# Performance work log

Measured on AMD Instinct MI355X. Metric: run time of the kernel, lower is better.

## Reference

```python
import jax, jax.numpy as jnp
import numpy as np

N_USER = 805   # herbs
N_ITEM = 390   # symptoms
N = 1195       # total nodes
D = 64         # embedding_dim (forced by final matmul)
E = 1_000_000
E_SUB = 500_000
B = 2048
BN_EPS = 1e-5


def _gcn(x, W, b, edge):
    # GCNConv_SH: message = Linear(x_j), aggr='mean', then tanh.
    # Linear commutes with mean (bias included when in-degree>0; isolated nodes -> 0),
    # so transform nodes once, then gather->segment-mean.
    h = x @ W.T + b                      # [N, D]
    src, dst = edge[0], edge[1]
    agg = jax.ops.segment_sum(h[src], dst, num_segments=N)          # [N, D]
    cnt = jax.ops.segment_sum(jnp.ones(edge.shape[1], x.dtype), dst, num_segments=N)
    mean = agg / jnp.maximum(cnt, 1.0)[:, None]   # isolated nodes stay 0 (PyG mean aggr)
    return jnp.tanh(mean)


def _two_layer(x, W1, b1, W2, b2, edge):
    return _gcn(_gcn(x, W1, b1, edge), W2, b2, edge)


def _norm(x, axis):
    # self.Norm(emb, count, n_dim): L2 normalize along n_dim (0 for user side, 1 for item side)
    return x / jnp.linalg.norm(x, axis=axis, keepdims=True)


def setup_inputs() -> dict:
    key = jax.random.key(0)
    ks = jax.random.split(key, 12)
    emb = jax.random.normal(ks[0], (N, D), jnp.float32)
    s = 1.0 / np.sqrt(D)
    W1 = jax.random.normal(ks[1], (D, D), jnp.float32) * s
    b1 = jnp.zeros((D,), jnp.float32)
    W2 = jax.random.normal(ks[2], (D, D), jnp.float32) * s
    b2 = jnp.zeros((D,), jnp.float32)
    mlp_W = jax.random.normal(ks[3], (64, D), jnp.float32) * s
    mlp_b = jnp.zeros((64,), jnp.float32)
    bn_gamma = jnp.ones((64,), jnp.float32)
    bn_beta = jnp.zeros((64,), jnp.float32)
    # multi-hot prescription; guarantee nonzero row sums for the mean-pool divide
    presc = (jax.random.uniform(ks[4], (B, N_ITEM)) < 0.05).astype(jnp.float32)
    presc = presc.at[:, 0].set(1.0)
    total_g = jax.random.randint(ks[5], (2, E), 0, N)
    sub_g1 = jax.random.randint(ks[6], (2, E_SUB), 0, N)
    sub_g2 = jax.random.randint(ks[7], (2, E_SUB), 0, N)
    edge_index_SH = jax.random.randint(ks[8], (2, 1000), 0, N)
    return {"edge_index_SH": edge_index_SH, "prescription": presc,
            "emb": emb, "W1": W1, "b1": b1, "W2": W2, "b2": b2,
            "mlp_W": mlp_W, "mlp_b": mlp_b, "bn_gamma": bn_gamma, "bn_beta": bn_beta,
            "total_g": total_g, "sub_g1": sub_g1, "sub_g2": sub_g2}


def reference(edge_index_SH, prescription, emb, W1, b1, W2, b2, mlp_W, mlp_b,
              bn_gamma, bn_beta, total_g, sub_g1, sub_g2):
    # edge_index_SH is accepted (forward signature) but unused, as in the source.
    x_SH1 = emb                                   # SH_embedding(arange(1195))
    x_SH6 = _two_layer(emb, W1, b1, W2, b2, total_g)   # two shared GCNConv_SH layers
    SH_g3 = _two_layer(emb, W1, b1, W2, b2, sub_g1)
    SH_g33 = _two_layer(emb, W1, b1, W2, b2, sub_g2)

    # ssl_layer_loss returns normalized previous (raw-embedding) views
    s_u = _norm(x_SH1[:N_USER], 0)   # [805, D]
    s_i = _norm(x_SH1[N_USER:], 1)   # [390, D]
    # sgl_loss returns normalized sub-graph-1 views
    n_u = _norm(SH_g3[:N_USER], 0)
    n_i = _norm(SH_g3[N_USER:], 1)
    # Same2Loss (reconstructed): fuse all contrastive views into final node reps
    c_u = 0.25 * (s_i + n_i + _norm(x_SH6[N_USER:], 1) + _norm(SH_g33[N_USER:], 1))  # [390, D]
    c_i = 0.25 * (s_u + n_u + _norm(x_SH6[:N_USER], 0) + _norm(SH_g33[:N_USER], 0))  # [805, D]

    e_synd = prescription @ c_u                           # [B, D]
    e_synd = e_synd / prescription.sum(axis=1, keepdims=True)
    h = e_synd @ mlp_W.T + mlp_b                          # [B, 64]
    mu = h.mean(axis=0)
    var = h.var(axis=0)                                   # biased, as torch BN training
    h = (h - mu) / jnp.sqrt(var + BN_EPS) * bn_gamma + bn_beta
    h = jax.nn.relu(h)
    pre = h @ c_i.T                                       # [B, 805]
    return pre
```

## Files before the change

kernel.cpp:

```cpp
#include <hip/hip_runtime.h>
#include <hip/hip_bf16.h>


#define NN    1195
#define NUSER 805
#define NITEM 390
#define DD    64
#define BB    2048
#define NPAD  1216
#define E_TOT 1000000
#define E_SUB 500000
#define MT    19
#define KT    8
#define CHUNK 3
#define LSTR  72
#define OUT2STRIDE (NN*DD)
#define CPG    299
#define P8W    152
#define FNT    13
#define KPAD   448
#define ENT    7

typedef unsigned int uint;
typedef unsigned short u16;
typedef unsigned char u8;
typedef __attribute__((ext_vector_type(8))) short short8;
typedef __attribute__((ext_vector_type(4))) float f32x4;

__device__ __forceinline__ float wsum(float v) {
#pragma unroll
    for (int m = 32; m > 0; m >>= 1) v += __shfl_xor(v, m, 64);
    return v;
}
__device__ __forceinline__ u16 f2b(float f) {
    uint u = __float_as_uint(f);
    return (u16)((u + 0x7FFFu + ((u >> 16) & 1u)) >> 16);
}
__device__ __forceinline__ float b2f16(u16 b) { return __uint_as_float(((uint)b) << 16); }
__device__ __forceinline__ void split4(const float* v, u16* hh, u16* ll) {
#pragma unroll
    for (int j = 0; j < 4; ++j) {
        u16 h = f2b(v[j]);
        hh[j] = h;
        ll[j] = f2b(v[j] - b2f16(h));
    }
}
__device__ __forceinline__ uint2 pack4(const u16* x) {
    uint2 o;
    o.x = (uint)x[0] | ((uint)x[1] << 16);
    o.y = (uint)x[2] | ((uint)x[3] << 16);
    return o;
}

#define CVT_EMB   0
#define CVT_W1    76480
#define CVT_B1    80576
#define CVT_W2    80640
#define CVT_B2    84736
#define CVT_MLPW  84800
#define CVT_MLPB  88896
#define CVT_GAMMA 88960
#define CVT_BETA  89024
#define CVT_TOTAL 89088

constexpr size_t alignUp64(size_t x) { return (x + 63) & ~size_t(63); }
constexpr size_t OFF_BNS  = 0;
constexpr size_t OFF_CNSS = 128;
constexpr size_t OFF_FLAG = 384;
constexpr size_t OFF_CVT  = 448;
constexpr size_t OFF_ABF  = alignUp64(OFF_CVT + CVT_TOTAL);
constexpr size_t OFF_RC   = alignUp64(OFF_ABF + (3ull * NN * NPAD) / 2);
constexpr size_t OFF_POOL = alignUp64(OFF_RC + 3ull * NPAD);


__global__ __launch_bounds__(1024, 8) void k_front(const void* presc, const void* emb,
        const void* p1, const void* p2, const void* p3, const void* p4,
        const void* p5, const void* p6, const void* p7, const void* p8, const void* p9,
        const int* __restrict__ tg, const int* __restrict__ s1, const int* __restrict__ s2,
        float* __restrict__ dst, float* __restrict__ cnss, float* __restrict__ bnsum,
        int* __restrict__ flag, uint* __restrict__ P8,
        int S0, int S1, int R, int rows, int HB) {
    extern __shared__ __align__(16) uint lds[];
    int b = blockIdx.x, t = threadIdx.x;
    int isbf = (((const u16*)presc)[0] == 0x3F80u) ? 1 : 0;
    if (b < HB) {
        int RS0 = R * S0, RS1 = R * S1;
        int g, p, r;
        if (b < RS0)            { g = 0; p = b % S0; r = b / S0; }
        else if (b < RS0 + RS1) { int b2 = b - RS0;        g = 1; p = b2 % S1; r = b2 / S1; }
        else                    { int b3 = b - RS0 - RS1;  g = 2; p = b3 % S1; r = b3 / S1; }
        int Sg = g ? S1 : S0;
        int cb = (g == 0) ? 0 : S0 + (g - 1) * S1;
        int r0 = r * rows;
        int nw4 = (rows * P8W) >> 2;
        {
            uint4* l4 = (uint4*)lds;
            for (int i = t; i < nw4; i += 1024) l4[i] = (uint4){0u, 0u, 0u, 0u};
        }
        __syncthreads();
        const int* eg = (g == 0) ? tg : (g == 1 ? s1 : s2);
        int Eg = (g == 0) ? E_TOT : E_SUB;
        int e0 = (int)(((long)p * Eg / Sg) & ~3L);
        int e1 = (p == Sg - 1) ? Eg : (int)(((long)(p + 1) * Eg / Sg) & ~3L);
        const int* srcp = eg;
        const int* dstp = eg + Eg;
        for (int i = e0 + t * 4; i < e1; i += 1024 * 4) {
            int4 d4 = *(const int4*)(dstp + i);
            int4 s4 = *(const int4*)(srcp + i);
            int rw;
            rw = d4.x - r0; if ((unsigned)rw < (unsigned)rows) atomicAdd(&lds[rw * P8W + (s4.x >> 3)], 1u << ((s4.x & 7) * 4));
            rw = d4.y - r0; if ((unsigned)rw < (unsigned)rows) atomicAdd(&lds[rw * P8W + (s4.y >> 3)], 1u << ((s4.y & 7) * 4));
            rw = d4.z - r0; if ((unsigned)rw < (unsigned)rows) atomicAdd(&lds[rw * P8W + (s4.z >> 3)], 1u << ((s4.z & 7) * 4));
            rw = d4.w - r0; if ((unsigned)rw < (unsigned)rows) atomicAdd(&lds[rw * P8W + (s4.w >> 3)], 1u << ((s4.w & 7) * 4));
        }
        __syncthreads();
        int rmax = rows; if (r0 + rmax > NN) rmax = NN - r0;
        uint* out = P8 + ((size_t)(cb + p) * NN + r0) * P8W;
        int n4 = (rmax * P8W) >> 2;
        const uint4* l4 = (const uint4*)lds;
        uint4* o4 = (uint4*)out;
        for (int i = t; i < n4; i += 1024) o4[i] = l4[i];
    } else if (b == HB) {
        if (t < 192) cnss[64 + t] = 0.0f;
        if (t < 128) bnsum[t] = 0.0f;
        int c = t & 63, chunk = t >> 6;
        float s = 0.0f;
        const u16* e16 = (const u16*)emb;
        const float* e32 = (const float*)emb;
        for (int r = chunk; r < NUSER; r += 16) {
            float v = isbf ? b2f16(e16[r * 64 + c]) : e32[r * 64 + c];
            s = fmaf(v, v, s);
        }
        float* sd = (float*)lds;
        sd[t] = s;
        __syncthreads();
        if (t < 64) {
            float tot = 0.0f;
#pragma unroll
            for (int j = 0; j < 16; ++j) tot += sd[j * 64 + t];
            cnss[t] = tot;
        }
    } else {
        int i = (b - HB - 1) * 1024 + t;
        if (i == 0) *flag = isbf;
        if (i < CVT_TOTAL) {
            const void* s2p; int o2;
            if      (i < CVT_W1)    { s2p = p1; o2 = i; }
            else if (i < CVT_B1)    { s2p = p2; o2 = i - CVT_W1; }
            else if (i < CVT_W2)    { s2p = p3; o2 = i - CVT_B1; }
            else if (i < CVT_B2)    { s2p = p4; o2 = i - CVT_W2; }
            else if (i < CVT_MLPW)  { s2p = p5; o2 = i - CVT_B2; }
            else if (i < CVT_MLPB)  { s2p = p6; o2 = i - CVT_MLPW; }
            else if (i < CVT_GAMMA) { s2p = p7; o2 = i - CVT_MLPB; }
            else if (i < CVT_BETA)  { s2p = p8; o2 = i - CVT_GAMMA; }
            else                    { s2p = p9; o2 = i - CVT_BETA; }
            dst[i] = isbf ? __bfloat162float(((const __hip_bfloat16*)s2p)[o2])
                          : ((const float*)s2p)[o2];
        }
    }
}

__device__ __forceinline__ void xf2_body(int g, int n0, int t,
        const float* xsrc, size_t xgstride,
        const float* part, const float* rcnt, int fromPart, int rowlim,
        const float* W, const float* bias,
        u16* Hhi, u16* Hlo, size_t hgstride, int ostride,
        u16* Ah, u16* Al, u16* Bh, u16* Bl, float* bs) {
    int w = t >> 6, l = t & 63;
    if (t < 64) bs[t] = bias ? bias[t] : 0.0f;
    int r = t >> 2, c0 = (t & 3) * 16;
    {
        const float* Wr = W + r * 64 + c0;
        float av[16];
#pragma unroll
        for (int j4 = 0; j4 < 4; ++j4) {
            float4 v = *(const float4*)(Wr + j4 * 4);
            av[j4*4+0] = v.x; av[j4*4+1] = v.y; av[j4*4+2] = v.z; av[j4*4+3] = v.w;
        }
#pragma unroll
        for (int j4 = 0; j4 < 4; ++j4) {
            u16 hh[4], ll[4];
            split4(av + j4*4, hh, ll);
            *(uint2*)(Ah + r * LSTR + c0 + j4*4) = pack4(hh);
            *(uint2*)(Al + r * LSTR + c0 + j4*4) = pack4(ll);
        }
    }
    {
        int node = n0 + r;
        float xr[16];
#pragma unroll
        for (int j = 0; j < 16; ++j) xr[j] = 0.0f;
        if (node < rowlim) {
            if (fromPart) {
#pragma unroll
                for (int k = 0; k < KT; ++k) {
                    const float* pp = part + (((size_t)k * 3 + g) * NPAD + node) * 64 + c0;
#pragma unroll
                    for (int j4 = 0; j4 < 4; ++j4) {
                        float4 v = *(const float4*)(pp + j4 * 4);
                        xr[j4*4+0] += v.x; xr[j4*4+1] += v.y;
                        xr[j4*4+2] += v.z; xr[j4*4+3] += v.w;
                    }
                }
                float rc = rcnt[g * NPAD + node];
#pragma unroll
                for (int j = 0; j < 16; ++j) xr[j] = tanhf(xr[j] * rc);
            } else {
                const float* Xr = xsrc + xgstride * g + (size_t)node * 64 + c0;
#pragma unroll
                for (int j4 = 0; j4 < 4; ++j4) {
                    float4 v = *(const float4*)(Xr + j4 * 4);
                    xr[j4*4+0] = v.x; xr[j4*4+1] = v.y;
                    xr[j4*4+2] = v.z; xr[j4*4+3] = v.w;
                }
            }
        }
#pragma unroll
        for (int j4 = 0; j4 < 4; ++j4) {
            u16 hh[4], ll[4];
            split4(xr + j4*4, hh, ll);
            *(uint2*)(Bh + r * LSTR + c0 + j4*4) = pack4(hh);
            *(uint2*)(Bl + r * LSTR + c0 + j4*4) = pack4(ll);
        }
    }
    __syncthreads();
    f32x4 acc[4];
#pragma unroll
    for (int p = 0; p < 4; ++p) acc[p] = (f32x4){0.f, 0.f, 0.f, 0.f};
    int mrow = w * 16 + (l & 15);
    int q8 = (l >> 4) * 8;
#pragma unroll
    for (int ks = 0; ks < 2; ++ks) {
        short8 ah = *(const short8*)(Ah + mrow * LSTR + ks * 32 + q8);
        short8 al = *(const short8*)(Al + mrow * LSTR + ks * 32 + q8);
#pragma unroll
        for (int p = 0; p < 4; ++p) {
            int nrow = p * 16 + (l & 15);
            short8 bh = *(const short8*)(Bh + nrow * LSTR + ks * 32 + q8);
            short8 bl = *(const short8*)(Bl + nrow * LSTR + ks * 32 + q8);
            acc[p] = __builtin_amdgcn_mfma_f32_16x16x32_bf16(ah, bh, acc[p], 0, 0, 0);
            acc[p] = __builtin_amdgcn_mfma_f32_16x16x32_bf16(ah, bl, acc[p], 0, 0, 0);
            acc[p] = __builtin_amdgcn_mfma_f32_16x16x32_bf16(al, bh, acc[p], 0, 0, 0);
        }
    }
    int q = l >> 4;
#pragma unroll
    for (int p = 0; p < 4; ++p) {
        int node = n0 + p * 16 + (l & 15);
#pragma unroll
        for (int rr2 = 0; rr2 < 4; ++rr2) {
            int d = w * 16 + q * 4 + rr2;
            float v = acc[p][rr2] + bs[d];
            u16 h = f2b(v);
            size_t o = hgstride * g + (size_t)d * ostride + node;
            Hhi[o] = h;
            Hlo[o] = f2b(v - b2f16(h));
        }
    }
}

__global__ __launch_bounds__(256) void k_xf2(const float* __restrict__ xsrc,
        size_t xgstride, const float* __restrict__ part, const float* __restrict__ rcnt,
        int fromPart, int ngb, int rowlim,
        const float* __restrict__ W, const float* __restrict__ bias,
        u16* __restrict__ Hhi, u16* __restrict__ Hlo, size_t hgstride, int ostride) {
    __shared__ u16 Ah[64 * LSTR], Al[64 * LSTR], Bh[64 * LSTR], Bl[64 * LSTR];
    __shared__ float bs[64];
    int b = blockIdx.x;
    xf2_body(b / ngb, (b % ngb) * 64, threadIdx.x, xsrc, xgstride, part, rcnt,
             fromPart, rowlim, W, bias, Hhi, Hlo, hgstride, ostride,
             Ah, Al, Bh, Bl, bs);
}

__global__ __launch_bounds__(256) void k_abf_xf1(const uint* __restrict__ P8,
        int S0, int S1,
        u16* __restrict__ Abf, float* __restrict__ rcnt,
        const float* __restrict__ embF, const float* __restrict__ W1,
        const float* __restrict__ b1, u16* __restrict__ H1hi, u16* __restrict__ H1lo) {
    __shared__ u16 Ah[64 * LSTR], Al[64 * LSTR], Bh[64 * LSTR], Bl[64 * LSTR];
    __shared__ float bs[64];
    __shared__ float ws4[4];
    int b = blockIdx.x, t = threadIdx.x;
    if (b < 3 * NN) {
        int g = b / NN, m = b % NN;
        int Sg = g ? S1 : S0;
        int cb = (g == 0) ? 0 : S0 + (g - 1) * S1;
        int w = t >> 6;
        float partial = 0.0f;
        if (t < P8W) {
            uint cnt[8] = {0, 0, 0, 0, 0, 0, 0, 0};
            for (int p = 0; p < Sg; ++p) {
                uint v = P8[((size_t)(cb + p) * NN + m) * P8W + t];
#pragma unroll
                for (int k = 0; k < 8; ++k) cnt[k] += (v >> (4 * k)) & 15u;
            }
            uint4 o;
            o.x = (uint)f2b((float)cnt[0]) | ((uint)f2b((float)cnt[1]) << 16);
            o.y = (uint)f2b((float)cnt[2]) | ((uint)f2b((float)cnt[3]) << 16);
            o.z = (uint)f2b((float)cnt[4]) | ((uint)f2b((float)cnt[5]) << 16);
            o.w = (uint)f2b((float)cnt[6]) | ((uint)f2b((float)cnt[7]) << 16);
            *(uint4*)(Abf + (size_t)b * NPAD + t * 8) = o;
#pragma unroll
            for (int k = 0; k < 8; ++k) partial += (float)cnt[k];
        }
        partial = wsum(partial);
        if ((t & 63) == 0) ws4[w] = partial;
        __syncthreads();
        if (t == 0)
            rcnt[g * NPAD + m] = 1.0f / fmaxf(ws4[0] + ws4[1] + ws4[2] + ws4[3], 1.0f);
    } else {
        int nt = b - 3 * NN;
        xf2_body(0, nt * 64, t, embF, 0, nullptr, nullptr, 0, NN, W1, b1,
                 H1hi, H1lo, 0, NPAD, Ah, Al, Bh, Bl, bs);
    }
}

__global__ __launch_bounds__(256) void k_aggp(const u16* __restrict__ Abf,
        const u16* __restrict__ Hhi, const u16* __restrict__ Hlo, size_t hstride,
        float* __restrict__ part) {
    int b = blockIdx.x;
    int kt = b & 7;
    int mt = (b >> 3) % MT;
    int g  = (b >> 3) / MT;
    int t = threadIdx.x, w = t >> 6, l = t & 63;
    __shared__ u16 As[64 * LSTR], Bh[64 * LSTR], Bl[64 * LSTR];
    f32x4 acc[4];
#pragma unroll
    for (int p = 0; p < 4; ++p) acc[p] = (f32x4){0.f, 0.f, 0.f, 0.f};
    int m0 = mt * 64;
    const u16* Ag = Abf + (size_t)g * NN * NPAD;
    const u16* Hg = Hhi + hstride * g;
    const u16* Lg = Hlo + hstride * g;
    int st0 = kt * CHUNK;
    int st1 = st0 + CHUNK; if (st1 > MT) st1 = MT;
    int rr = t >> 4, c4 = (t & 15) * 4;
    for (int st = st0; st < st1; ++st) {
        int s0 = st * 64;
        __syncthreads();
#pragma unroll
        for (int pass = 0; pass < 4; ++pass) {
            int r = pass * 16 + rr;
            uint2 av = {0u, 0u};
            if (m0 + r < NN) av = *(const uint2*)(Ag + (size_t)(m0 + r) * NPAD + s0 + c4);
            *(uint2*)(As + r * LSTR + c4) = av;
            *(uint2*)(Bh + r * LSTR + c4) = *(const uint2*)(Hg + (size_t)r * NPAD + s0 + c4);
            *(uint2*)(Bl + r * LSTR + c4) = *(const uint2*)(Lg + (size_t)r * NPAD + s0 + c4);
        }
        __syncthreads();
        int mrow = w * 16 + (l & 15);
        int q8 = (l >> 4) * 8;
#pragma unroll
        for (int ks = 0; ks < 2; ++ks) {
            short8 a = *(const short8*)(As + mrow * LSTR + ks * 32 + q8);
#pragma unroll
            for (int p = 0; p < 4; ++p) {
                int nrow = p * 16 + (l & 15);
                short8 bh = *(const short8*)(Bh + nrow * LSTR + ks * 32 + q8);
                short8 bl = *(const short8*)(Bl + nrow * LSTR + ks * 32 + q8);
                acc[p] = __builtin_amdgcn_mfma_f32_16x16x32_bf16(a, bh, acc[p], 0, 0, 0);
                acc[p] = __builtin_amdgcn_mfma_f32_16x16x32_bf16(a, bl, acc[p], 0, 0, 0);
            }
        }
    }
    int q = l >> 4;
#pragma unroll
    for (int p = 0; p < 4; ++p) {
        int n = p * 16 + (l & 15);
#pragma unroll
        for (int r = 0; r < 4; ++r) {
            int m = m0 + w * 16 + q * 4 + r;
            if (m < NN)
                part[(((size_t)kt * 3 + g) * NPAD + m) * 64 + n] = acc[p][r];
        }
    }
}

__global__ __launch_bounds__(256) void k_comb(const float* __restrict__ part,
        const float* __restrict__ rcnt, float* __restrict__ out, float* __restrict__ cnss) {
    int g = blockIdx.x / CPG, bi = blockIdx.x % CPG;
    int t = threadIdx.x;
    int idx = bi * 256 + t;
    int m = idx >> 6, n = idx & 63;
    bool valid = idx < NN * 64;
    float v = 0.0f;
    if (valid) {
        float s = 0.0f;
#pragma unroll
        for (int k = 0; k < KT; ++k)
            s += part[(((size_t)k * 3 + g) * NPAD + m) * 64 + n];
        v = tanhf(s * rcnt[g * NPAD + m]);
        out[(size_t)g * NN * 64 + idx] = v;
    }
    float x2 = (valid && m < NUSER) ? v * v : 0.0f;
    __shared__ float sd[256];
    sd[t] = x2;
    __syncthreads();
    if (t < 64) {
        float s = sd[t] + sd[t + 64] + sd[t + 128] + sd[t + 192];
        if (s != 0.0f) atomicAdd(&cnss[(g + 1) * 64 + t], s);
    }
}

__global__ void k_cuci(const float* __restrict__ embf, const float* __restrict__ out2,
                       const float* __restrict__ cnss, float* __restrict__ cu,
                       float* __restrict__ ci) {
    int b = blockIdx.x, l = threadIdx.x;
    if (b < 448) {
        if (b >= NITEM) { cu[(size_t)b * DD + l] = 0.0f; return; }
        int node = NUSER + b;
        const float* v0 = embf + (size_t)node * DD;
        const float* v1 = out2 + (size_t)node * DD;
        const float* v2 = out2 + OUT2STRIDE + (size_t)node * DD;
        const float* v3 = out2 + 2ull * OUT2STRIDE + (size_t)node * DD;
        float total = 0.0f;
        { float x = v0[l]; float ss = wsum(x * x); total += x / sqrtf(ss); }
        { float x = v1[l]; float ss = wsum(x * x); total += x / sqrtf(ss); }
        { float x = v2[l]; float ss = wsum(x * x); total += x / sqrtf(ss); }
        { float x = v3[l]; float ss = wsum(x * x); total += x / sqrtf(ss); }
        cu[(size_t)b * DD + l] = 0.25f * total;
    } else {
        int u = b - 448;
        size_t i = (size_t)u * DD + l;
        float s = embf[i] / sqrtf(cnss[l])
                + out2[i] / sqrtf(cnss[64 + l])
                + out2[OUT2STRIDE + i] / sqrtf(cnss[128 + l])
                + out2[2ull * OUT2STRIDE + i] / sqrtf(cnss[192 + l]);
        ci[i] = 0.25f * s;
    }
}

__global__ __launch_bounds__(256) void k_esynd(const void* __restrict__ presc,
        const u16* __restrict__ cwh, const u16* __restrict__ cwl,
        const float* __restrict__ mlpB, const int* __restrict__ flag,
        float* __restrict__ hpre, float* __restrict__ bnsum) {
    int m0 = blockIdx.x * 64;
    int t = threadIdx.x, w = t >> 6, l = t & 63;
    int isbf = *flag;
    const u16* pB = (const u16*)presc;
    const float* pF = (const float*)presc;
    __shared__ u16 As[64 * LSTR], Bh[64 * LSTR], Bl[64 * LSTR];
    __shared__ u16 Ones[16 * LSTR];
    __shared__ float bs[64];
    __shared__ float r1[4][64], r2[4][64];
    for (int i = t; i < 16 * LSTR; i += 256) Ones[i] = (i < 64) ? 0x3F80u : 0u;
    if (t < 64) bs[t] = mlpB[t];

    f32x4 acc[4], acc1;
#pragma unroll
    for (int p = 0; p < 4; ++p) acc[p] = (f32x4){0.f, 0.f, 0.f, 0.f};
    acc1 = (f32x4){0.f, 0.f, 0.f, 0.f};

    int rr = t >> 4, c4 = (t & 15) * 4;
    for (int st = 0; st < ENT; ++st) {
        int s0 = st * 64;
        __syncthreads();
#pragma unroll
        for (int pass = 0; pass < 4; ++pass) {
            int r = pass * 16 + rr;
            int m = m0 + r;
            int kb = s0 + c4;
            u16 a4[4];
            if (kb + 3 < NITEM) {
                if (isbf) {
                    const uint* p32 = (const uint*)pB + (((size_t)m * NITEM + kb) >> 1);
                    uint u0 = p32[0], u1 = p32[1];
                    a4[0] = (u16)u0; a4[1] = (u16)(u0 >> 16);
                    a4[2] = (u16)u1; a4[3] = (u16)(u1 >> 16);
                } else {
                    const float2* pf2 = (const float2*)(pF + (size_t)m * NITEM + kb);
                    float2 f0 = pf2[0], f1 = pf2[1];
                    a4[0] = f2b(f0.x); a4[1] = f2b(f0.y);
                    a4[2] = f2b(f1.x); a4[3] = f2b(f1.y);
                }
            } else {
#pragma unroll
                for (int j = 0; j < 4; ++j) {
                    int k = kb + j;
                    a4[j] = (k < NITEM)
                          ? (isbf ? pB[(size_t)m * NITEM + k] : f2b(pF[(size_t)m * NITEM + k]))
                          : (u16)0;
                }
            }
            uint2 o;
            o.x = (uint)a4[0] | ((uint)a4[1] << 16);
            o.y = (uint)a4[2] | ((uint)a4[3] << 16);
            *(uint2*)(As + r * LSTR + c4) = o;
            *(uint2*)(Bh + r * LSTR + c4) = *(const uint2*)(cwh + (size_t)r * KPAD + s0 + c4);
            *(uint2*)(Bl + r * LSTR + c4) = *(const uint2*)(cwl + (size_t)r * KPAD + s0 + c4);
        }
        __syncthreads();
        int mrow = w * 16 + (l & 15);
        int q8 = (l >> 4) * 8;
#pragma unroll
        for (int ks = 0; ks < 2; ++ks) {
            short8 a = *(const short8*)(As + mrow * LSTR + ks * 32 + q8);
            short8 on = *(const short8*)(Ones + (l & 15) * LSTR + ks * 32 + q8);
            acc1 = __builtin_amdgcn_mfma_f32_16x16x32_bf16(a, on, acc1, 0, 0, 0);
#pragma unroll
            for (int p = 0; p < 4; ++p) {
                int nrow = p * 16 + (l & 15);
                short8 bh = *(const short8*)(Bh + nrow * LSTR + ks * 32 + q8);
                short8 bl = *(const short8*)(Bl + nrow * LSTR + ks * 32 + q8);
                acc[p] = __builtin_amdgcn_mfma_f32_16x16x32_bf16(a, bh, acc[p], 0, 0, 0);
                acc[p] = __builtin_amdgcn_mfma_f32_16x16x32_bf16(a, bl, acc[p], 0, 0, 0);
            }
        }
    }
    float inv[4];
#pragma unroll
    for (int r = 0; r < 4; ++r)
        inv[r] = 1.0f / __shfl(acc1[r], l & 48, 64);
    int q = l >> 4;
#pragma unroll
    for (int p = 0; p < 4; ++p) {
        int col = p * 16 + (l & 15);
        float a = 0.0f, c = 0.0f;
#pragma unroll
        for (int r = 0; r < 4; ++r) {
            float hv = acc[p][r] * inv[r] + bs[col];
            hpre[(size_t)(m0 + w * 16 + q * 4 + r) * DD + col] = hv;
            a += hv; c = fmaf(hv, hv, c);
        }
        a += __shfl_xor(a, 16, 64); a += __shfl_xor(a, 32, 64);
        c += __shfl_xor(c, 16, 64); c += __shfl_xor(c, 32, 64);
        if (l < 16) { r1[w][col] = a; r2[w][col] = c; }
    }
    __syncthreads();
    if (t < 64) {
        atomicAdd(&bnsum[t],      r1[0][t] + r1[1][t] + r1[2][t] + r1[3][t]);
        atomicAdd(&bnsum[64 + t], r2[0][t] + r2[1][t] + r2[2][t] + r2[3][t]);
    }
}

__global__ __launch_bounds__(256) void k_final(const float* __restrict__ hpre,
        const float* __restrict__ bnsum, const float* __restrict__ gamma,
        const float* __restrict__ beta, const float* __restrict__ ci,
        void* __restrict__ out, const int* __restrict__ flag) {
    int b = blockIdx.x;
    int mt = b / FNT, nt = b % FNT;
    int m0 = mt * 64, n0 = nt * 64;
    int t = threadIdx.x, w = t >> 6, l = t & 63;
    __shared__ u16 Ah[64 * LSTR], Al[64 * LSTR], Bh[64 * LSTR], Bl[64 * LSTR];
    __shared__ float mn[64], rsg[64], bt[64];
    if (t < 64) {
        float mean = bnsum[t] * (1.0f / BB);
        float var = bnsum[64 + t] * (1.0f / BB) - mean * mean;
        mn[t] = mean;
        rsg[t] = gamma[t] / sqrtf(var + 1e-5f);
        bt[t] = beta[t];
    }
    __syncthreads();
    const float4* hp4 = (const float4*)(hpre + (size_t)m0 * 64);
    const float4* ci4 = (const float4*)ci;
#pragma unroll
    for (int k = 0; k < 4; ++k) {
        int i = t + k * 256;
        int r = i >> 4, c4 = (i & 15) * 4;
        float4 v = hp4[i];
        float vv[4] = {v.x, v.y, v.z, v.w};
        u16 hh[4], ll[4];
#pragma unroll
        for (int j = 0; j < 4; ++j) {
            int d = c4 + j;
            float x = fmaxf((vv[j] - mn[d]) * rsg[d] + bt[d], 0.0f);
            u16 hb = f2b(x);
            hh[j] = hb;
            ll[j] = f2b(x - b2f16(hb));
        }
        *(uint2*)(Ah + r * LSTR + c4) = pack4(hh);
        *(uint2*)(Al + r * LSTR + c4) = pack4(ll);
        int col = n0 + r;
        float4 cv = (col < NUSER) ? ci4[(size_t)col * 16 + (i & 15)]
                                  : (float4){0.f, 0.f, 0.f, 0.f};
        float cc[4] = {cv.x, cv.y, cv.z, cv.w};
        split4(cc, hh, ll);
        *(uint2*)(Bh + r * LSTR + c4) = pack4(hh);
        *(uint2*)(Bl + r * LSTR + c4) = pack4(ll);
    }
    __syncthreads();
    f32x4 acc[4];
#pragma unroll
    for (int p = 0; p < 4; ++p) acc[p] = (f32x4){0.f, 0.f, 0.f, 0.f};
    int mrow = w * 16 + (l & 15);
    int q8 = (l >> 4) * 8;
#pragma unroll
    for (int ks = 0; ks < 2; ++ks) {
        short8 ah = *(const short8*)(Ah + mrow * LSTR + ks * 32 + q8);
        short8 al = *(const short8*)(Al + mrow * LSTR + ks * 32 + q8);
#pragma unroll
        for (int p = 0; p < 4; ++p) {
            int nrow = p * 16 + (l & 15);
            short8 bh = *(const short8*)(Bh + nrow * LSTR + ks * 32 + q8);
            short8 bl = *(const short8*)(Bl + nrow * LSTR + ks * 32 + q8);
            acc[p] = __builtin_amdgcn_mfma_f32_16x16x32_bf16(ah, bh, acc[p], 0, 0, 0);
            acc[p] = __builtin_amdgcn_mfma_f32_16x16x32_bf16(ah, bl, acc[p], 0, 0, 0);
            acc[p] = __builtin_amdgcn_mfma_f32_16x16x32_bf16(al, bh, acc[p], 0, 0, 0);
        }
    }
    int isbf = *flag;
    int q = l >> 4;
#pragma unroll
    for (int p = 0; p < 4; ++p) {
        int col = n0 + p * 16 + (l & 15);
        if (col < NUSER) {
#pragma unroll
            for (int r = 0; r < 4; ++r) {
                int row = m0 + w * 16 + q * 4 + r;
                size_t o = (size_t)row * NUSER + col;
                if (isbf) ((__hip_bfloat16*)out)[o] = __float2bfloat16(acc[p][r]);
                else      ((float*)out)[o] = acc[p][r];
            }
        }
    }
}

extern "C" void kernel_launch(void* const* d_in, const int* in_sizes, int n_in,
                              void* d_out, int out_size, void* d_ws, size_t ws_size,
                              hipStream_t stream) {
    const void* presc = d_in[1];
    const void* emb   = d_in[2];
    const void* W1    = d_in[3];
    const void* b1    = d_in[4];
    const void* W2    = d_in[5];
    const void* b2    = d_in[6];
    const void* mlpW  = d_in[7];
    const void* mlpB  = d_in[8];
    const void* gamma = d_in[9];
    const void* beta  = d_in[10];
    const int* tg = (const int*)d_in[11];
    const int* s1 = (const int*)d_in[12];
    const int* s2 = (const int*)d_in[13];
    float* ws = (float*)d_ws;
    (void)in_sizes; (void)n_in; (void)out_size;

    float* bnsum = ws + OFF_BNS;
    float* cnss  = ws + OFF_CNSS;
    int*   flag  = (int*)(ws + OFF_FLAG);
    float* cvt   = ws + OFF_CVT;
    float* embF  = cvt + CVT_EMB;
    float* W1F   = cvt + CVT_W1;
    float* b1F   = cvt + CVT_B1;
    float* W2F   = cvt + CVT_W2;
    float* b2F   = cvt + CVT_B2;
    float* mlpWF = cvt + CVT_MLPW;
    float* mlpBF = cvt + CVT_MLPB;
    float* gamF  = cvt + CVT_GAMMA;
    float* betF  = cvt + CVT_BETA;
    u16*   Abf   = (u16*)(ws + OFF_ABF);
    float* rcnt  = ws + OFF_RC;
    uint*  P8    = (uint*)(ws + OFF_POOL);
    float* part  = ws + OFF_POOL;
    u16*   cwh   = (u16*)(ws + OFF_POOL);
    u16*   cwl   = cwh + 64ull * KPAD;

    static int g_rows = 0;
    if (g_rows == 0) {
        hipError_t e = hipFuncSetAttribute((const void*)k_front,
                hipFuncAttributeMaxDynamicSharedMemorySize, 128 * P8W * 4);
        g_rows = (e == hipSuccess) ? 128 : 96;
    }
    int rows = g_rows;
    int R = (NN + rows - 1) / rows;

    size_t cpw = (size_t)NN * P8W;
    size_t tailF = 760000;
    int SU = 1;
    if      ((OFF_POOL + 32 * cpw + tailF) * 4 <= ws_size) SU = 4;
    else if ((OFF_POOL + 16 * cpw + tailF) * 4 <= ws_size) SU = 2;
    int S0 = 4 * SU, S1 = 2 * SU;
    int copies = S0 + 2 * S1;

    size_t o = alignUp64(OFF_POOL + (size_t)copies * cpw);
    u16*   H1hi = (u16*)(ws + o);  u16* H1lo = H1hi + 64ull * NPAD;
    o = alignUp64(o + 64ull * NPAD);
    u16*   H2hi = (u16*)(ws + o);  u16* H2lo = H2hi + 3ull * 64 * NPAD;
    o = alignUp64(o + 3ull * 64 * NPAD);
    float* out2 = ws + o;          o = alignUp64(o + 3ull * NN * DD);
    float* cu   = ws + o;          o = alignUp64(o + 448ull * DD);
    float* ci   = ws + o;          o = alignUp64(o + (size_t)NUSER * DD);
    float* hpre = ws + o;

    int HB = R * copies;
    int CVTB = CVT_TOTAL / 1024;

    k_front<<<HB + 1 + CVTB, 1024, rows * P8W * 4, stream>>>(presc, emb,
        emb, W1, b1, W2, b2, mlpW, mlpB, gamma, beta,
        tg, s1, s2, cvt, cnss, bnsum, flag, P8, S0, S1, R, rows, HB);
    k_abf_xf1<<<3 * NN + MT, 256, 0, stream>>>(P8, S0, S1, Abf, rcnt,
        embF, W1F, b1F, H1hi, H1lo);
    k_aggp<<<3 * MT * KT, 256, 0, stream>>>(Abf, H1hi, H1lo, 0, part);
    k_xf2<<<3 * MT, 256, 0, stream>>>(nullptr, 0, part, rcnt, 1, MT, NN,
        W2F, b2F, H2hi, H2lo, 64ull * NPAD, NPAD);
    k_aggp<<<3 * MT * KT, 256, 0, stream>>>(Abf, H2hi, H2lo, 64ull * NPAD, part);
    k_comb<<<3 * CPG, 256, 0, stream>>>(part, rcnt, out2, cnss);
    k_cuci<<<448 + NUSER, 64, 0, stream>>>(embF, out2, cnss, cu, ci);
    k_xf2<<<ENT, 256, 0, stream>>>(cu, 0, nullptr, nullptr, 0, ENT, 448,
        mlpWF, nullptr, cwh, cwl, 0, KPAD);
    k_esynd<<<BB / 64, 256, 0, stream>>>(presc, cwh, cwl, mlpBF, flag, hpre, bnsum);
    k_final<<<(BB / 64) * FNT, 256, 0, stream>>>(hpre, bnsum, gamF, betF, ci, d_out, flag);
}
```

Before: 197.7 us.

## Fuse GCN aggregation with tanh/transform and combine, dropping split-K partials

The split-K aggregation (8 K-chunks writing float partials) plus separate xf2 and comb kernels is replaced by two fused kernels. Each runs the full K loop per 64-row tile. The first applies tanh, mean scaling and the W2 transform in-block. The second applies tanh, writes out2 and accumulates column sums of squares. This removes partial-buffer traffic and two launches, but cuts grid size from 456 blocks to 57 per aggregation, so each block runs a 19-step serial K loop with less parallelism. k_cuci is also repacked to four nodes per 256-thread block.

```diff
diff --git a/kernel.cpp b/kernel.cpp
--- a/kernel.cpp
+++ b/kernel.cpp
@@ -11,15 +11,13 @@
 #define E_TOT 1000000
 #define E_SUB 500000
 #define MT    19
-#define KT    8
-#define CHUNK 3
 #define LSTR  72
 #define OUT2STRIDE (NN*DD)
-#define CPG    299
 #define P8W    152
 #define FNT    13
 #define KPAD   448
 #define ENT    7
+#define CUCIB  ((448 + NUSER + 3) / 4)
 
 typedef unsigned int uint;
 typedef unsigned short u16;
@@ -72,6 +70,7 @@
 constexpr size_t OFF_RC   = alignUp64(OFF_ABF + (3ull * NN * NPAD) / 2);
 constexpr size_t OFF_POOL = alignUp64(OFF_RC + 3ull * NPAD);
 
+#define SM_BYTES 37632
 
 __global__ __launch_bounds__(1024, 8) void k_front(const void* presc, const void* emb,
         const void* p1, const void* p2, const void* p3, const void* p4,
@@ -160,11 +159,41 @@
     }
 }
 
-__device__ __forceinline__ void xf2_body(int g, int n0, int t,
-        const float* xsrc, size_t xgstride,
-        const float* part, const float* rcnt, int fromPart, int rowlim,
+
+__device__ __forceinline__ void merge_body(int b, int t, const uint* P8, int S0, int S1,
+        u16* Abf, float* rcnt, float* ws4) {
+    int g = b / NN, m = b % NN;
+    int Sg = g ? S1 : S0;
+    int cb = (g == 0) ? 0 : S0 + (g - 1) * S1;
+    int w = t >> 6;
+    float partial = 0.0f;
+    if (t < P8W) {
+        uint cnt[8] = {0, 0, 0, 0, 0, 0, 0, 0};
+        for (int p = 0; p < Sg; ++p) {
+            uint v = P8[((size_t)(cb + p) * NN + m) * P8W + t];
+#pragma unroll
+            for (int k = 0; k < 8; ++k) cnt[k] += (v >> (4 * k)) & 15u;
+        }
+        uint4 o;
+        o.x = (uint)f2b((float)cnt[0]) | ((uint)f2b((float)cnt[1]) << 16);
+        o.y = (uint)f2b((float)cnt[2]) | ((uint)f2b((float)cnt[3]) << 16);
+        o.z = (uint)f2b((float)cnt[4]) | ((uint)f2b((float)cnt[5]) << 16);
+        o.w = (uint)f2b((float)cnt[6]) | ((uint)f2b((float)cnt[7]) << 16);
+        *(uint4*)(Abf + (size_t)b * NPAD + t * 8) = o;
+#pragma unroll
+        for (int k = 0; k < 8; ++k) partial += (float)cnt[k];
+    }
+    partial = wsum(partial);
+    if ((t & 63) == 0) ws4[w] = partial;
+    __syncthreads();
+    if (t == 0)
+        rcnt[g * NPAD + m] = 1.0f / fmaxf(ws4[0] + ws4[1] + ws4[2] + ws4[3], 1.0f);
+}
+
+__device__ __forceinline__ void xf2_body(int n0, int t,
+        const float* xsrc, int rowlim,
         const float* W, const float* bias,
-        u16* Hhi, u16* Hlo, size_t hgstride, int ostride,
+        u16* Hhi, u16* Hlo, int ostride,
         u16* Ah, u16* Al, u16* Bh, u16* Bl, float* bs) {
     int w = t >> 6, l = t & 63;
     if (t < 64) bs[t] = bias ? bias[t] : 0.0f;
@@ -191,28 +220,12 @@
 #pragma unroll
         for (int j = 0; j < 16; ++j) xr[j] = 0.0f;
         if (node < rowlim) {
-            if (fromPart) {
-#pragma unroll
-                for (int k = 0; k < KT; ++k) {
-                    const float* pp = part + (((size_t)k * 3 + g) * NPAD + node) * 64 + c0;
-#pragma unroll
-                    for (int j4 = 0; j4 < 4; ++j4) {
-                        float4 v = *(const float4*)(pp + j4 * 4);
-                        xr[j4*4+0] += v.x; xr[j4*4+1] += v.y;
-                        xr[j4*4+2] += v.z; xr[j4*4+3] += v.w;
-                    }
-                }
-                float rc = rcnt[g * NPAD + node];
-#pragma unroll
-                for (int j = 0; j < 16; ++j) xr[j] = tanhf(xr[j] * rc);
-            } else {
-                const float* Xr = xsrc + xgstride * g + (size_t)node * 64 + c0;
-#pragma unroll
-                for (int j4 = 0; j4 < 4; ++j4) {
-                    float4 v = *(const float4*)(Xr + j4 * 4);
-                    xr[j4*4+0] = v.x; xr[j4*4+1] = v.y;
-                    xr[j4*4+2] = v.z; xr[j4*4+3] = v.w;
-                }
+            const float* Xr = xsrc + (size_t)node * 64 + c0;
+#pragma unroll
+            for (int j4 = 0; j4 < 4; ++j4) {
+                float4 v = *(const float4*)(Xr + j4 * 4);
+                xr[j4*4+0] = v.x; xr[j4*4+1] = v.y;
+                xr[j4*4+2] = v.z; xr[j4*4+3] = v.w;
             }
         }
 #pragma unroll
@@ -252,89 +265,22 @@
             int d = w * 16 + q * 4 + rr2;
             float v = acc[p][rr2] + bs[d];
             u16 h = f2b(v);
-            size_t o = hgstride * g + (size_t)d * ostride + node;
+            size_t o = (size_t)d * ostride + node;
             Hhi[o] = h;
             Hlo[o] = f2b(v - b2f16(h));
         }
     }
 }
 
-__global__ __launch_bounds__(256) void k_xf2(const float* __restrict__ xsrc,
-        size_t xgstride, const float* __restrict__ part, const float* __restrict__ rcnt,
-        int fromPart, int ngb, int rowlim,
-        const float* __restrict__ W, const float* __restrict__ bias,
-        u16* __restrict__ Hhi, u16* __restrict__ Hlo, size_t hgstride, int ostride) {
-    __shared__ u16 Ah[64 * LSTR], Al[64 * LSTR], Bh[64 * LSTR], Bl[64 * LSTR];
-    __shared__ float bs[64];
-    int b = blockIdx.x;
-    xf2_body(b / ngb, (b % ngb) * 64, threadIdx.x, xsrc, xgstride, part, rcnt,
-             fromPart, rowlim, W, bias, Hhi, Hlo, hgstride, ostride,
-             Ah, Al, Bh, Bl, bs);
-}
-
-__global__ __launch_bounds__(256) void k_abf_xf1(const uint* __restrict__ P8,
-        int S0, int S1,
-        u16* __restrict__ Abf, float* __restrict__ rcnt,
-        const float* __restrict__ embF, const float* __restrict__ W1,
-        const float* __restrict__ b1, u16* __restrict__ H1hi, u16* __restrict__ H1lo) {
-    __shared__ u16 Ah[64 * LSTR], Al[64 * LSTR], Bh[64 * LSTR], Bl[64 * LSTR];
-    __shared__ float bs[64];
-    __shared__ float ws4[4];
-    int b = blockIdx.x, t = threadIdx.x;
-    if (b < 3 * NN) {
-        int g = b / NN, m = b % NN;
-        int Sg = g ? S1 : S0;
-        int cb = (g == 0) ? 0 : S0 + (g - 1) * S1;
-        int w = t >> 6;
-        float partial = 0.0f;
-        if (t < P8W) {
-            uint cnt[8] = {0, 0, 0, 0, 0, 0, 0, 0};
-            for (int p = 0; p < Sg; ++p) {
-                uint v = P8[((size_t)(cb + p) * NN + m) * P8W + t];
-#pragma unroll
-                for (int k = 0; k < 8; ++k) cnt[k] += (v >> (4 * k)) & 15u;
-            }
-            uint4 o;
-            o.x = (uint)f2b((float)cnt[0]) | ((uint)f2b((float)cnt[1]) << 16);
-            o.y = (uint)f2b((float)cnt[2]) | ((uint)f2b((float)cnt[3]) << 16);
-            o.z = (uint)f2b((float)cnt[4]) | ((uint)f2b((float)cnt[5]) << 16);
-            o.w = (uint)f2b((float)cnt[6]) | ((uint)f2b((float)cnt[7]) << 16);
-            *(uint4*)(Abf + (size_t)b * NPAD + t * 8) = o;
-#pragma unroll
-            for (int k = 0; k < 8; ++k) partial += (float)cnt[k];
-        }
-        partial = wsum(partial);
-        if ((t & 63) == 0) ws4[w] = partial;
-        __syncthreads();
-        if (t == 0)
-            rcnt[g * NPAD + m] = 1.0f / fmaxf(ws4[0] + ws4[1] + ws4[2] + ws4[3], 1.0f);
-    } else {
-        int nt = b - 3 * NN;
-        xf2_body(0, nt * 64, t, embF, 0, nullptr, nullptr, 0, NN, W1, b1,
-                 H1hi, H1lo, 0, NPAD, Ah, Al, Bh, Bl, bs);
-    }
-}
-
-__global__ __launch_bounds__(256) void k_aggp(const u16* __restrict__ Abf,
-        const u16* __restrict__ Hhi, const u16* __restrict__ Hlo, size_t hstride,
-        float* __restrict__ part) {
-    int b = blockIdx.x;
-    int kt = b & 7;
-    int mt = (b >> 3) % MT;
-    int g  = (b >> 3) / MT;
-    int t = threadIdx.x, w = t >> 6, l = t & 63;
-    __shared__ u16 As[64 * LSTR], Bh[64 * LSTR], Bl[64 * LSTR];
-    f32x4 acc[4];
+__device__ __forceinline__ void agg_full(int g, int m0, int t,
+        const u16* Abf, const u16* Hg, const u16* Lg,
+        u16* As, u16* Sh, u16* Sl, f32x4* acc) {
 #pragma unroll
     for (int p = 0; p < 4; ++p) acc[p] = (f32x4){0.f, 0.f, 0.f, 0.f};
-    int m0 = mt * 64;
+    int w = t >> 6, l = t & 63;
     const u16* Ag = Abf + (size_t)g * NN * NPAD;
-    const u16* Hg = Hhi + hstride * g;
-    const u16* Lg = Hlo + hstride * g;
-    int st0 = kt * CHUNK;
-    int st1 = st0 + CHUNK; if (st1 > MT) st1 = MT;
     int rr = t >> 4, c4 = (t & 15) * 4;
-    for (int st = st0; st < st1; ++st) {
+    for (int st = 0; st < MT; ++st) {
         int s0 = st * 64;
         __syncthreads();
 #pragma unroll
@@ -343,8 +289,8 @@
             uint2 av = {0u, 0u};
             if (m0 + r < NN) av = *(const uint2*)(Ag + (size_t)(m0 + r) * NPAD + s0 + c4);
             *(uint2*)(As + r * LSTR + c4) = av;
-            *(uint2*)(Bh + r * LSTR + c4) = *(const uint2*)(Hg + (size_t)r * NPAD + s0 + c4);
-            *(uint2*)(Bl + r * LSTR + c4) = *(const uint2*)(Lg + (size_t)r * NPAD + s0 + c4);
+            *(uint2*)(Sh + r * LSTR + c4) = *(const uint2*)(Hg + (size_t)r * NPAD + s0 + c4);
+            *(uint2*)(Sl + r * LSTR + c4) = *(const uint2*)(Lg + (size_t)r * NPAD + s0 + c4);
         }
         __syncthreads();
         int mrow = w * 16 + (l & 15);
@@ -355,56 +301,156 @@
 #pragma unroll
             for (int p = 0; p < 4; ++p) {
                 int nrow = p * 16 + (l & 15);
-                short8 bh = *(const short8*)(Bh + nrow * LSTR + ks * 32 + q8);
-                short8 bl = *(const short8*)(Bl + nrow * LSTR + ks * 32 + q8);
+                short8 bh = *(const short8*)(Sh + nrow * LSTR + ks * 32 + q8);
+                short8 bl = *(const short8*)(Sl + nrow * LSTR + ks * 32 + q8);
                 acc[p] = __builtin_amdgcn_mfma_f32_16x16x32_bf16(a, bh, acc[p], 0, 0, 0);
                 acc[p] = __builtin_amdgcn_mfma_f32_16x16x32_bf16(a, bl, acc[p], 0, 0, 0);
             }
         }
     }
+}
+
+
+__global__ __launch_bounds__(256) void k_agg1xf2(const u16* __restrict__ Abf,
+        const u16* __restrict__ H1hi, const u16* __restrict__ H1lo,
+        const float* __restrict__ rcnt, const float* __restrict__ W2,
+        const float* __restrict__ b2, u16* __restrict__ H2hi, u16* __restrict__ H2lo) {
+    int b = blockIdx.x;
+    int g = b / MT, mt = b % MT;
+    int m0 = mt * 64;
+    int t = threadIdx.x, w = t >> 6, l = t & 63;
+    __shared__ u16 As[64 * LSTR], Sh[64 * LSTR], Sl[64 * LSTR];
+    __shared__ u16 Wh[64 * LSTR], Wl[64 * LSTR];
+    __shared__ u16 Xh[64 * LSTR], Xl[64 * LSTR];
+    __shared__ float bs[64];
+    if (t < 64) bs[t] = b2[t];
+    {
+        int r = t >> 2, c0 = (t & 3) * 16;
+        const float* Wr = W2 + r * 64 + c0;
+#pragma unroll
+        for (int j4 = 0; j4 < 4; ++j4) {
+            float4 v = *(const float4*)(Wr + j4 * 4);
+            float a4[4] = {v.x, v.y, v.z, v.w};
+            u16 hh[4], ll[4];
+            split4(a4, hh, ll);
+            *(uint2*)(Wh + r * LSTR + c0 + j4 * 4) = pack4(hh);
+            *(uint2*)(Wl + r * LSTR + c0 + j4 * 4) = pack4(ll);
+        }
+    }
+    f32x4 acc[4];
+    agg_full(g, m0, t, Abf, H1hi, H1lo, As, Sh, Sl, acc);
     int q = l >> 4;
 #pragma unroll
     for (int p = 0; p < 4; ++p) {
         int n = p * 16 + (l & 15);
 #pragma unroll
-        for (int r = 0; r < 4; ++r) {
-            int m = m0 + w * 16 + q * 4 + r;
-            if (m < NN)
-                part[(((size_t)kt * 3 + g) * NPAD + m) * 64 + n] = acc[p][r];
-        }
-    }
-}
-
-__global__ __launch_bounds__(256) void k_comb(const float* __restrict__ part,
-        const float* __restrict__ rcnt, float* __restrict__ out, float* __restrict__ cnss) {
-    int g = blockIdx.x / CPG, bi = blockIdx.x % CPG;
-    int t = threadIdx.x;
-    int idx = bi * 256 + t;
-    int m = idx >> 6, n = idx & 63;
-    bool valid = idx < NN * 64;
-    float v = 0.0f;
-    if (valid) {
-        float s = 0.0f;
-#pragma unroll
-        for (int k = 0; k < KT; ++k)
-            s += part[(((size_t)k * 3 + g) * NPAD + m) * 64 + n];
-        v = tanhf(s * rcnt[g * NPAD + m]);
-        out[(size_t)g * NN * 64 + idx] = v;
-    }
-    float x2 = (valid && m < NUSER) ? v * v : 0.0f;
-    __shared__ float sd[256];
-    sd[t] = x2;
+        for (int r2 = 0; r2 < 4; ++r2) {
+            int lm = w * 16 + q * 4 + r2;
+            int m = m0 + lm;
+            float rc = (m < NN) ? rcnt[g * NPAD + m] : 0.0f;
+            float v = tanhf(acc[p][r2] * rc);
+            u16 h = f2b(v);
+            Xh[lm * LSTR + n] = h;
+            Xl[lm * LSTR + n] = f2b(v - b2f16(h));
+        }
+    }
     __syncthreads();
-    if (t < 64) {
-        float s = sd[t] + sd[t + 64] + sd[t + 128] + sd[t + 192];
-        if (s != 0.0f) atomicAdd(&cnss[(g + 1) * 64 + t], s);
-    }
-}
-
-__global__ void k_cuci(const float* __restrict__ embf, const float* __restrict__ out2,
-                       const float* __restrict__ cnss, float* __restrict__ cu,
-                       float* __restrict__ ci) {
-    int b = blockIdx.x, l = threadIdx.x;
+    f32x4 acc2[4];
+#pragma unroll
+    for (int p = 0; p < 4; ++p) acc2[p] = (f32x4){0.f, 0.f, 0.f, 0.f};
+    int mrow = w * 16 + (l & 15);
+    int q8 = (l >> 4) * 8;
+#pragma unroll
+    for (int ks = 0; ks < 2; ++ks) {
+        short8 ah = *(const short8*)(Wh + mrow * LSTR + ks * 32 + q8);
+        short8 al = *(const short8*)(Wl + mrow * LSTR + ks * 32 + q8);
+#pragma unroll
+        for (int p = 0; p < 4; ++p) {
+            int nrow = p * 16 + (l & 15);
+            short8 bh = *(const short8*)(Xh + nrow * LSTR + ks * 32 + q8);
+            short8 bl = *(const short8*)(Xl + nrow * LSTR + ks * 32 + q8);
+            acc2[p] = __builtin_amdgcn_mfma_f32_16x16x32_bf16(ah, bh, acc2[p], 0, 0, 0);
+            acc2[p] = __builtin_amdgcn_mfma_f32_16x16x32_bf16(ah, bl, acc2[p], 0, 0, 0);
+            acc2[p] = __builtin_amdgcn_mfma_f32_16x16x32_bf16(al, bh, acc2[p], 0, 0, 0);
+        }
+    }
+#pragma unroll
+    for (int p = 0; p < 4; ++p) {
+        int node = m0 + p * 16 + (l & 15);
+#pragma unroll
+        for (int r2 = 0; r2 < 4; ++r2) {
+            int d = w * 16 + q * 4 + r2;
+            float v = acc2[p][r2] + bs[d];
+            u16 h = f2b(v);
+            size_t o = (size_t)g * 64 * NPAD + (size_t)d * NPAD + node;
+            H2hi[o] = h;
+            H2lo[o] = f2b(v - b2f16(h));
+        }
+    }
+}
+
+__global__ __launch_bounds__(256) void k_agg2comb(const u16* __restrict__ Abf,
+        const u16* __restrict__ H2hi, const u16* __restrict__ H2lo,
+        const float* __restrict__ rcnt, float* __restrict__ out2,
+        float* __restrict__ cnss) {
+    int b = blockIdx.x;
+    int g = b / MT, mt = b % MT;
+    int m0 = mt * 64;
+    int t = threadIdx.x, w = t >> 6, l = t & 63;
+    __shared__ u16 As[64 * LSTR], Sh[64 * LSTR], Sl[64 * LSTR];
+    __shared__ float cn[64];
+    if (t < 64) cn[t] = 0.0f;
+    f32x4 acc[4];
+    agg_full(g, m0, t, Abf, H2hi + (size_t)g * 64 * NPAD, H2lo + (size_t)g * 64 * NPAD,
+             As, Sh, Sl, acc);
+    int q = l >> 4;
+#pragma unroll
+    for (int p = 0; p < 4; ++p) {
+        int n = p * 16 + (l & 15);
+        float colsum = 0.0f;
+#pragma unroll
+        for (int r2 = 0; r2 < 4; ++r2) {
+            int m = m0 + w * 16 + q * 4 + r2;
+            if (m < NN) {
+                float v = tanhf(acc[p][r2] * rcnt[g * NPAD + m]);
+                out2[((size_t)g * NN + m) * 64 + n] = v;
+                if (m < NUSER) colsum = fmaf(v, v, colsum);
+            }
+        }
+        if (colsum != 0.0f) atomicAdd(&cn[n], colsum);
+    }
+    __syncthreads();
+    if (t < 64 && cn[t] != 0.0f) atomicAdd(&cnss[(g + 1) * 64 + t], cn[t]);
+}
+
+__global__ __launch_bounds__(256) void k_abf_xf1(const uint* __restrict__ P8,
+        int S0, int S1, u16* __restrict__ Abf, float* __restrict__ rcnt,
+        const float* __restrict__ embF, const float* __restrict__ W1,
+        const float* __restrict__ b1, u16* __restrict__ H1hi, u16* __restrict__ H1lo) {
+    __shared__ __align__(16) u8 smem[SM_BYTES];
+    int b = blockIdx.x, t = threadIdx.x;
+    if (b < 3 * NN)
+        merge_body(b, t, P8, S0, S1, Abf, rcnt, (float*)smem);
+    else
+        xf2_body((b - 3 * NN) * 64, t, embF, NN, W1, b1, H1hi, H1lo, NPAD,
+                 (u16*)smem, (u16*)(smem + 9216), (u16*)(smem + 18432),
+                 (u16*)(smem + 27648), (float*)(smem + 36864));
+}
+__global__ __launch_bounds__(256) void k_xf2(const float* __restrict__ xsrc,
+        int rowlim, const float* __restrict__ W, const float* __restrict__ bias,
+        u16* __restrict__ Hhi, u16* __restrict__ Hlo, int ostride) {
+    __shared__ __align__(16) u8 smem[SM_BYTES];
+    xf2_body(blockIdx.x * 64, threadIdx.x, xsrc, rowlim, W, bias, Hhi, Hlo, ostride,
+             (u16*)smem, (u16*)(smem + 9216), (u16*)(smem + 18432),
+             (u16*)(smem + 27648), (float*)(smem + 36864));
+}
+
+__global__ __launch_bounds__(256) void k_cuci(const float* __restrict__ embf,
+        const float* __restrict__ out2, const float* __restrict__ cnss,
+        float* __restrict__ cu, float* __restrict__ ci) {
+    int b = blockIdx.x * 4 + (threadIdx.x >> 6);
+    int l = threadIdx.x & 63;
+    if (b >= 448 + NUSER) return;
     if (b < 448) {
         if (b >= NITEM) { cu[(size_t)b * DD + l] = 0.0f; return; }
         int node = NUSER + b;
@@ -649,7 +695,6 @@
     u16*   Abf   = (u16*)(ws + OFF_ABF);
     float* rcnt  = ws + OFF_RC;
     uint*  P8    = (uint*)(ws + OFF_POOL);
-    float* part  = ws + OFF_POOL;
     u16*   cwh   = (u16*)(ws + OFF_POOL);
     u16*   cwl   = cwh + 64ull * KPAD;
 
@@ -661,7 +706,6 @@
     }
     int rows = g_rows;
     int R = (NN + rows - 1) / rows;
-
     size_t cpw = (size_t)NN * P8W;
     size_t tailF = 760000;
     int SU = 1;
@@ -681,21 +725,18 @@
     float* hpre = ws + o;
 
     int HB = R * copies;
-    int CVTB = CVT_TOTAL / 1024;
+    int CVTB = (CVT_TOTAL + 1023) / 1024;
 
     k_front<<<HB + 1 + CVTB, 1024, rows * P8W * 4, stream>>>(presc, emb,
         emb, W1, b1, W2, b2, mlpW, mlpB, gamma, beta,
         tg, s1, s2, cvt, cnss, bnsum, flag, P8, S0, S1, R, rows, HB);
     k_abf_xf1<<<3 * NN + MT, 256, 0, stream>>>(P8, S0, S1, Abf, rcnt,
         embF, W1F, b1F, H1hi, H1lo);
-    k_aggp<<<3 * MT * KT, 256, 0, stream>>>(Abf, H1hi, H1lo, 0, part);
-    k_xf2<<<3 * MT, 256, 0, stream>>>(nullptr, 0, part, rcnt, 1, MT, NN,
-        W2F, b2F, H2hi, H2lo, 64ull * NPAD, NPAD);
-    k_aggp<<<3 * MT * KT, 256, 0, stream>>>(Abf, H2hi, H2lo, 64ull * NPAD, part);
-    k_comb<<<3 * CPG, 256, 0, stream>>>(part, rcnt, out2, cnss);
-    k_cuci<<<448 + NUSER, 64, 0, stream>>>(embF, out2, cnss, cu, ci);
-    k_xf2<<<ENT, 256, 0, stream>>>(cu, 0, nullptr, nullptr, 0, ENT, 448,
-        mlpWF, nullptr, cwh, cwl, 0, KPAD);
+    k_agg1xf2<<<3 * MT, 256, 0, stream>>>(Abf, H1hi, H1lo, rcnt, W2F, b2F, H2hi, H2lo);
+    k_agg2comb<<<3 * MT, 256, 0, stream>>>(Abf, H2hi, H2lo, rcnt, out2, cnss);
+    k_cuci<<<CUCIB, 256, 0, stream>>>(embF, out2, cnss, cu, ci);
+    k_xf2<<<ENT, 256, 0, stream>>>(cu, 448, mlpWF, nullptr, cwh, cwl, KPAD);
     k_esynd<<<BB / 64, 256, 0, stream>>>(presc, cwh, cwl, mlpBF, flag, hpre, bnsum);
-    k_final<<<(BB / 64) * FNT, 256, 0, stream>>>(hpre, bnsum, gamF, betF, ci, d_out, flag);
-}
+    k_final<<<(BB / 64) * FNT, 256, 0, stream>>>(hpre, bnsum, gamF, betF, ci,
+        d_out, flag);
+}
```

After: 250.9 us. 1.27x slower.
